# Kernel optimization log

Hardware: AMD Instinct MI355X
Metric: run time of the kernel (lower is better)

The kernel has to match this reference:

```python
import jax, jax.numpy as jnp
from jax import lax
import numpy as np

SEQ, IN, H, C = 8192, 256, 2048, 2


def setup_inputs() -> dict:
    key = jax.random.key(0)
    ks = jax.random.split(key, 9)
    s = 1.0 / np.sqrt(H)
    u = lambda k, shape: jax.random.uniform(k, shape, jnp.float32, -s, s)
    return {
        "x": jax.random.normal(ks[0], (SEQ, 1, IN), jnp.float32),
        "h0": jax.random.normal(ks[1], (H,), jnp.float32),
        "c0": jax.random.normal(ks[2], (H,), jnp.float32),
        "w_ih": u(ks[3], (4 * H, IN)),
        "w_hh": u(ks[4], (4 * H, H)),
        "b_ih": u(ks[5], (4 * H,)),
        "b_hh": u(ks[6], (4 * H,)),
        "w_lin": u(ks[7], (C, H)),
        "b_lin": u(ks[8], (C,)),
    }


def _lstm_last_h(xs, h0, c0, w_ih, w_hh, b_ih, b_hh):
    # Precompute input contributions for all steps in one GEMM: (SEQ, 4H)
    xg = xs @ w_ih.T + (b_ih + b_hh)

    def step(carry, xg_t):
        h, c = carry
        g = xg_t + w_hh @ h  # (4H,)
        i, f, gc, o = jnp.split(g, 4)
        i = jax.nn.sigmoid(i)
        f = jax.nn.sigmoid(f)
        gc = jnp.tanh(gc)
        o = jax.nn.sigmoid(o)
        c = f * c + i * gc
        h = o * jnp.tanh(c)
        return (h, c), None

    (h, _c), _ = lax.scan(step, (h0, c0), xg)
    return h


def reference(x, h0, c0, w_ih, w_hh, b_ih, b_hh, w_lin, b_lin):
    xs = x[:, 0, :]  # (SEQ, IN), batch dim of 1 squeezed
    h = _lstm_last_h(xs, h0, c0, w_ih, w_hh, b_ih, b_hh)  # (H,)
    logit = h @ w_lin.T + b_lin  # (C,)
    return logit[None, :]  # (1, C), matching output.squeeze(dim=1) @ linear
```

## Files before the change

### kernel.cpp

```cpp
#include <hip/hip_runtime.h>
#include <math.h>

#define SEQ   8192
#define NIN   256
#define H     2048
#define NBLK  256
#define NTHR  256
#define NREP  16

typedef unsigned long long u64;


__global__ void lstm_init(const float* __restrict__ h0, float* __restrict__ ws)
{
    const int b = threadIdx.x;
    unsigned* tags = (unsigned*)(ws + 2 * H);
    #pragma unroll
    for (int r = 0; r < 8; ++r) {
        unsigned hv = __builtin_bit_cast(unsigned, h0[8 * b + r]);
        __hip_atomic_store((unsigned*)ws + 8 * b + r, hv,
                           __ATOMIC_RELAXED, __HIP_MEMORY_SCOPE_AGENT);
    }
    #pragma unroll
    for (int r = 0; r < NREP; ++r) {
        __hip_atomic_store(&tags[r * NBLK + b], 0u,
                           __ATOMIC_RELAXED, __HIP_MEMORY_SCOPE_AGENT);
        __hip_atomic_store(&tags[(NREP + r) * NBLK + b], 0xFFFFFFFFu,
                           __ATOMIC_RELAXED, __HIP_MEMORY_SCOPE_AGENT);
    }
}

__device__ __forceinline__ void wave_poll_tags(const u64* tp, unsigned t, int ln)
{
    const u64 want = ((u64)t << 32) | (u64)t;
    for (;;) {
        u64 a = __hip_atomic_load(tp + ln,      __ATOMIC_RELAXED, __HIP_MEMORY_SCOPE_AGENT);
        u64 b = __hip_atomic_load(tp + 64 + ln, __ATOMIC_RELAXED, __HIP_MEMORY_SCOPE_AGENT);
        if (__all((a == want) && (b == want))) break;
        __builtin_amdgcn_s_sleep(2);
    }
}

__global__ void __launch_bounds__(NTHR, 1)
lstm_persist(const float* __restrict__ x, const float* __restrict__ c0,
             const float* __restrict__ w_ih, const float* __restrict__ w_hh,
             const float* __restrict__ b_ih, const float* __restrict__ b_hh,
             const float* __restrict__ w_lin, const float* __restrict__ b_lin,
             float* __restrict__ out, float* __restrict__ ws)
{
    const int b = blockIdx.x, tid = threadIdx.x;
    const int wv = tid >> 6, ln = tid & 63;
    float*    hA   = ws;
    unsigned* tags = (unsigned*)(ws + 2 * H);
    const int rep  = b & (NREP - 1);

    __shared__ float  h_lds[H + H / 32];
    __shared__ double gsum[4][8];
    __shared__ double bias_s[4][8];
    __shared__ double red0[4], red1[4];

    if (tid < 32) {
        int g = tid >> 3, r = tid & 7;
        int R = g * H + b * 8 + r;
        bias_s[g][r] = (double)b_ih[R] + (double)b_hh[R];
    }
    double c_reg = (wv == 0 && ln < 8) ? (double)c0[b * 8 + ln] : 0.0;

    float wreg[8][32];
    float wih[8][4];
    #pragma unroll
    for (int r = 0; r < 8; ++r) {
        const int R = wv * H + b * 8 + r;
        const float4* wp = (const float4*)(w_hh + (size_t)R * H + ln * 32);
        #pragma unroll
        for (int q = 0; q < 8; ++q) ((float4*)wreg[r])[q] = wp[q];
        *(float4*)wih[r] = *(const float4*)(w_ih + (size_t)R * NIN + ln * 4);
    }
    __syncthreads();

    float4 xr = *(const float4*)(x + ln * 4);
    float4 xn = xr;

    for (int t = 0; t < SEQ; ++t) {
        const int slot = t & 1;

        if (t + 1 < SEQ) xn = *(const float4*)(x + (size_t)(t + 1) * NIN + ln * 4);

        if (wv == 0)
            wave_poll_tags((const u64*)(tags + (slot * NREP + rep) * NBLK),
                           (unsigned)t, ln);
        __syncthreads();

        __builtin_amdgcn_fence(__ATOMIC_ACQUIRE, "agent");
        {
            const float4* hp = (const float4*)(hA + slot * H) + tid * 2;
            float4 v0 = hp[0], v1 = hp[1];
            const int base = 8 * tid + (tid >> 2);
            h_lds[base + 0] = v0.x; h_lds[base + 1] = v0.y;
            h_lds[base + 2] = v0.z; h_lds[base + 3] = v0.w;
            h_lds[base + 4] = v1.x; h_lds[base + 5] = v1.y;
            h_lds[base + 6] = v1.z; h_lds[base + 7] = v1.w;
        }
        __syncthreads();

        float hbuf[32];
        {
            const float* hp = &h_lds[33 * ln];
            #pragma unroll
            for (int q = 0; q < 32; ++q) hbuf[q] = hp[q];
        }
        double acc[8];
        #pragma unroll
        for (int r = 0; r < 8; ++r)
            acc[r] = (double)wih[r][0] * (double)xr.x + (double)wih[r][1] * (double)xr.y
                   + (double)wih[r][2] * (double)xr.z + (double)wih[r][3] * (double)xr.w;
        #pragma unroll
        for (int q = 0; q < 32; ++q) {
            const double hq = (double)hbuf[q];
            #pragma unroll
            for (int r = 0; r < 8; ++r)
                acc[r] = fma((double)wreg[r][q], hq, acc[r]);
        }
        #pragma unroll
        for (int off = 32; off >= 1; off >>= 1) {
            #pragma unroll
            for (int r = 0; r < 8; ++r) acc[r] += __shfl_xor(acc[r], off, 64);
        }
        if (ln == 0) {
            #pragma unroll
            for (int r = 0; r < 8; ++r) gsum[wv][r] = acc[r];
        }
        __syncthreads();

        if (wv == 0) {
            double actv = 0.0;
            if (ln < 32) {
                const int g = ln >> 3, j = ln & 7;
                double v = gsum[g][j] + bias_s[g][j];
                actv = (g == 2) ? tanh(v) : 1.0 / (1.0 + exp(-v));
            }
            const int j = ln & 7;
            double ai = __shfl(actv, j,      64);
            double af = __shfl(actv, j + 8,  64);
            double ag = __shfl(actv, j + 16, 64);
            double ao = __shfl(actv, j + 24, 64);
            if (ln < 8) {
                double c = af * c_reg + ai * ag;
                c_reg = c;
                float hnew = (float)(ao * tanh(c));
                unsigned* dst = (unsigned*)(hA + (1 - slot) * H) + 8 * b + ln;
                __hip_atomic_store(dst, __builtin_bit_cast(unsigned, hnew),
                                   __ATOMIC_RELAXED, __HIP_MEMORY_SCOPE_AGENT);
            }
            asm volatile("s_waitcnt vmcnt(0)" ::: "memory");
            if (ln < NREP)
                __hip_atomic_store(&tags[((1 - slot) * NREP + ln) * NBLK + b],
                                   (unsigned)(t + 1),
                                   __ATOMIC_RELAXED, __HIP_MEMORY_SCOPE_AGENT);
        }
        xr = xn;
    }

    if (b == 0) {
        if (wv == 0) wave_poll_tags((const u64*)tags, (unsigned)SEQ, ln);
        __syncthreads();
        __builtin_amdgcn_fence(__ATOMIC_ACQUIRE, "agent");
        double a0 = 0., a1 = 0.;
        {
            const float4* hp = (const float4*)hA + tid * 2;
            float4 v0 = hp[0], v1 = hp[1];
            const float hv[8] = { v0.x, v0.y, v0.z, v0.w, v1.x, v1.y, v1.z, v1.w };
            #pragma unroll
            for (int q = 0; q < 8; ++q) {
                const int k = 8 * tid + q;
                a0 = fma((double)w_lin[k],     (double)hv[q], a0);
                a1 = fma((double)w_lin[H + k], (double)hv[q], a1);
            }
        }
        #pragma unroll
        for (int off = 32; off >= 1; off >>= 1) {
            a0 += __shfl_xor(a0, off, 64);
            a1 += __shfl_xor(a1, off, 64);
        }
        if (ln == 0) { red0[wv] = a0; red1[wv] = a1; }
        __syncthreads();
        if (tid == 0) {
            out[0] = (float)(red0[0] + red0[1] + red0[2] + red0[3] + (double)b_lin[0]);
            out[1] = (float)(red1[0] + red1[1] + red1[2] + red1[3] + (double)b_lin[1]);
        }
    }
}

extern "C" void kernel_launch(void* const* d_in, const int* in_sizes, int n_in,
                              void* d_out, int out_size, void* d_ws, size_t ws_size,
                              hipStream_t stream) {
    const float* x     = (const float*)d_in[0];
    const float* h0    = (const float*)d_in[1];
    const float* c0    = (const float*)d_in[2];
    const float* w_ih  = (const float*)d_in[3];
    const float* w_hh  = (const float*)d_in[4];
    const float* b_ih  = (const float*)d_in[5];
    const float* b_hh  = (const float*)d_in[6];
    const float* w_lin = (const float*)d_in[7];
    const float* b_lin = (const float*)d_in[8];
    float* out = (float*)d_out;
    float* ws  = (float*)d_ws;

    lstm_init<<<1, NTHR, 0, stream>>>(h0, ws);
    lstm_persist<<<NBLK, NTHR, 0, stream>>>(
        x, c0, w_ih, w_hh, b_ih, b_hh, w_lin, b_lin, out, ws);
}
```

Before: 216.5 ms.

## Use a ring of hidden-state slots with periodic acquire fences and single tag copy

Replaces the double-buffered hidden state with a K-slot ring sized from the workspace, so each block issues an agent-scope acquire fence only once every P steps, staggered across blocks. The 16 replicated tag arrays become one tag array that every block polls. The aim is to cut per-step cache-invalidate fences and tag-store traffic in the grid-wide step barrier. The risk is correctness: without a fence each step, stale cached h values may be read. Having all blocks poll the same tags may also add contention.

```diff
diff --git a/kernel.cpp b/kernel.cpp
--- a/kernel.cpp
+++ b/kernel.cpp
@@ -6,28 +6,18 @@
 #define H     2048
 #define NBLK  256
 #define NTHR  256
-#define NREP  16
 
 typedef unsigned long long u64;
 
 
-__global__ void lstm_init(const float* __restrict__ h0, float* __restrict__ ws)
+__global__ void lstm_init(const float* __restrict__ h0, float* __restrict__ hS,
+                          unsigned* __restrict__ tags)
 {
-    const int b = threadIdx.x;
-    unsigned* tags = (unsigned*)(ws + 2 * H);
+    const int j = threadIdx.x;
     #pragma unroll
-    for (int r = 0; r < 8; ++r) {
-        unsigned hv = __builtin_bit_cast(unsigned, h0[8 * b + r]);
-        __hip_atomic_store((unsigned*)ws + 8 * b + r, hv,
-                           __ATOMIC_RELAXED, __HIP_MEMORY_SCOPE_AGENT);
-    }
-    #pragma unroll
-    for (int r = 0; r < NREP; ++r) {
-        __hip_atomic_store(&tags[r * NBLK + b], 0u,
-                           __ATOMIC_RELAXED, __HIP_MEMORY_SCOPE_AGENT);
-        __hip_atomic_store(&tags[(NREP + r) * NBLK + b], 0xFFFFFFFFu,
-                           __ATOMIC_RELAXED, __HIP_MEMORY_SCOPE_AGENT);
-    }
+    for (int r = 0; r < 8; ++r) hS[8 * j + r] = h0[8 * j + r];
+    tags[j]        = 0u;
+    tags[NBLK + j] = 0xFFFFFFFFu;
 }
 
 __device__ __forceinline__ void wave_poll_tags(const u64* tp, unsigned t, int ln)
@@ -46,13 +36,12 @@
              const float* __restrict__ w_ih, const float* __restrict__ w_hh,
              const float* __restrict__ b_ih, const float* __restrict__ b_hh,
              const float* __restrict__ w_lin, const float* __restrict__ b_lin,
-             float* __restrict__ out, float* __restrict__ ws)
+             float* __restrict__ out, float* __restrict__ hS,
+             unsigned* __restrict__ tags, int K, int P)
 {
     const int b = blockIdx.x, tid = threadIdx.x;
     const int wv = tid >> 6, ln = tid & 63;
-    float*    hA   = ws;
-    unsigned* tags = (unsigned*)(ws + 2 * H);
-    const int rep  = b & (NREP - 1);
+    const u64* tagsU = (const u64*)tags;
 
     __shared__ float  h_lds[H + H / 32];
     __shared__ double gsum[4][8];
@@ -81,19 +70,21 @@
     float4 xr = *(const float4*)(x + ln * 4);
     float4 xn = xr;
 
+    int scur = 0;
+    int fcnt = (b % P) + 1;
+
     for (int t = 0; t < SEQ; ++t) {
-        const int slot = t & 1;
+        const int tagslot = t & 1;
+        const int snext = (scur + 1 == K) ? 0 : scur + 1;
 
         if (t + 1 < SEQ) xn = *(const float4*)(x + (size_t)(t + 1) * NIN + ln * 4);
 
         if (wv == 0)
-            wave_poll_tags((const u64*)(tags + (slot * NREP + rep) * NBLK),
-                           (unsigned)t, ln);
-        __syncthreads();
-
-        __builtin_amdgcn_fence(__ATOMIC_ACQUIRE, "agent");
+            wave_poll_tags(tagsU + tagslot * (NBLK / 2), (unsigned)t, ln);
+        __syncthreads();
+
         {
-            const float4* hp = (const float4*)(hA + slot * H) + tid * 2;
+            const float4* hp = (const float4*)(hS + (size_t)scur * H) + tid * 2;
             float4 v0 = hp[0], v1 = hp[1];
             const int base = 8 * tid + (tid >> 2);
             h_lds[base + 0] = v0.x; h_lds[base + 1] = v0.y;
@@ -102,6 +93,11 @@
             h_lds[base + 6] = v1.z; h_lds[base + 7] = v1.w;
         }
         __syncthreads();
+
+        if (--fcnt == 0) {
+            fcnt = P;
+            if (tid == 0) __builtin_amdgcn_fence(__ATOMIC_ACQUIRE, "agent");
+        }
 
         float hbuf[32];
         {
@@ -148,26 +144,27 @@
                 double c = af * c_reg + ai * ag;
                 c_reg = c;
                 float hnew = (float)(ao * tanh(c));
-                unsigned* dst = (unsigned*)(hA + (1 - slot) * H) + 8 * b + ln;
+                unsigned* dst = (unsigned*)(hS + (size_t)snext * H) + 8 * b + ln;
                 __hip_atomic_store(dst, __builtin_bit_cast(unsigned, hnew),
                                    __ATOMIC_RELAXED, __HIP_MEMORY_SCOPE_AGENT);
             }
             asm volatile("s_waitcnt vmcnt(0)" ::: "memory");
-            if (ln < NREP)
-                __hip_atomic_store(&tags[((1 - slot) * NREP + ln) * NBLK + b],
-                                   (unsigned)(t + 1),
+            if (ln == 0)
+                __hip_atomic_store(&tags[(1 - tagslot) * NBLK + b], (unsigned)(t + 1),
                                    __ATOMIC_RELAXED, __HIP_MEMORY_SCOPE_AGENT);
         }
         xr = xn;
+        scur = snext;
     }
 
     if (b == 0) {
-        if (wv == 0) wave_poll_tags((const u64*)tags, (unsigned)SEQ, ln);
-        __syncthreads();
-        __builtin_amdgcn_fence(__ATOMIC_ACQUIRE, "agent");
+        if (wv == 0) wave_poll_tags(tagsU, (unsigned)SEQ, ln);
+        __syncthreads();
+        if (tid == 0) __builtin_amdgcn_fence(__ATOMIC_ACQUIRE, "agent");
+        __syncthreads();
         double a0 = 0., a1 = 0.;
         {
-            const float4* hp = (const float4*)hA + tid * 2;
+            const float4* hp = (const float4*)(hS + (size_t)scur * H) + tid * 2;
             float4 v0 = hp[0], v1 = hp[1];
             const float hv[8] = { v0.x, v0.y, v0.z, v0.w, v1.x, v1.y, v1.z, v1.w };
             #pragma unroll
@@ -206,7 +203,15 @@
     float* out = (float*)d_out;
     float* ws  = (float*)d_ws;
 
-    lstm_init<<<1, NTHR, 0, stream>>>(h0, ws);
+    const size_t slotB = (size_t)H * 4, tagB = 2 * NBLK * 4;
+    int K = 2;
+    while (K < 1024 && ((size_t)(K * 2) * slotB + tagB) <= ws_size) K *= 2;
+    int P = K / 2; if (P < 1) P = 1;
+
+    float*    hS   = ws;
+    unsigned* tags = (unsigned*)(ws + (size_t)K * H);
+
+    lstm_init<<<1, NTHR, 0, stream>>>(h0, hS, tags);
     lstm_persist<<<NBLK, NTHR, 0, stream>>>(
-        x, c0, w_ih, w_hh, b_ih, b_hh, w_lin, b_lin, out, ws);
-}
+        x, c0, w_ih, w_hh, b_ih, b_hh, w_lin, b_lin, out, hS, tags, K, P);
+}
```

After: 180.3 ms. 1.2x faster.
